# Kernel optimization log

Measured on AMD Instinct MI355X. Metric: run time of the kernel, lower is better.

The kernel has to match this reference:

```python
import jax, jax.numpy as jnp
import numpy as np

NUM_GROUPS = 32
EPS = 1e-6
NUM_HEADS = 8
HEAD_DIM = 64


def group_norm(x, gamma, beta):
    # x: [B, C, H, W]
    B, C, H, W = x.shape
    xg = x.reshape(B, NUM_GROUPS, C // NUM_GROUPS, H, W)
    mean = xg.mean(axis=(2, 3, 4), keepdims=True)
    var = xg.var(axis=(2, 3, 4), keepdims=True)
    xn = ((xg - mean) * jax.lax.rsqrt(var + EPS)).reshape(B, C, H, W)
    return xn * gamma[None, :, None, None] + beta[None, :, None, None]


def setup_inputs() -> dict:
    key = jax.random.key(0)
    ks = jax.random.split(key, 4)
    B, C, H, W = 8, 512, 32, 32
    hid = NUM_HEADS * HEAD_DIM  # 512
    x = jax.random.normal(ks[0], (B, C, H, W), dtype=jnp.float32)
    gamma = jnp.ones((C,), dtype=jnp.float32)
    beta = jnp.zeros((C,), dtype=jnp.float32)
    w_in = jax.random.normal(ks[1], (3 * hid, C), dtype=jnp.float32) * (1.0 / np.sqrt(C))
    b_in = jnp.zeros((3 * hid,), dtype=jnp.float32)
    w_out = jax.random.normal(ks[2], (C, hid), dtype=jnp.float32) * (1.0 / np.sqrt(hid))
    b_out = jnp.zeros((C,), dtype=jnp.float32)
    return {"x": x, "gamma": gamma, "beta": beta, "w_in": w_in, "b_in": b_in,
            "w_out": w_out, "b_out": b_out}


def reference(x, gamma, beta, w_in, b_in, w_out, b_out):
    B, C, H, W = x.shape
    n, c = NUM_HEADS, HEAD_DIM
    skip = x
    h = group_norm(x, gamma, beta)
    # 1x1 conv proj_in: [B, 3*n*c, H, W]
    qkv = jnp.einsum('oc,bchw->bohw', w_in, h) + b_in[None, :, None, None]
    qkv = qkv.reshape(B, 3, n, c, H * W)
    q, k, v = qkv[:, 0], qkv[:, 1], qkv[:, 2]  # each [B, n, c, HW]
    scale = 1.0 / np.sqrt(c)
    logits = jnp.einsum('bncq,bnck->bnqk', q, k) * scale  # [B, n, HW, HW]
    w = jax.nn.softmax(logits, axis=-1)
    out = jnp.einsum('bnqk,bnck->bncq', w, v)  # [B, n, c, HW]
    out = out.reshape(B, n * c, H, W)
    out = jnp.einsum('oc,bchw->bohw', w_out, out) + b_out[None, :, None, None]
    return out + skip
```

## Files before the change

### kernel.cpp

```cpp
#include <hip/hip_runtime.h>
#include <hip/hip_bf16.h>

#define B_    8
#define C_    512
#define HW_   1024
#define NG    32
#define GCH   16
#define EPSV  1e-6f

typedef __attribute__((ext_vector_type(8))) short short8;
typedef __attribute__((ext_vector_type(4))) short short4v;
typedef __attribute__((ext_vector_type(4))) float floatx4;

static __device__ __forceinline__ short f2bs(float f) {
  return __builtin_bit_cast(short, __float2bfloat16(f));
}
static __device__ __forceinline__ short4v pack4(float a, float b, float c, float d) {
  return (short4v){f2bs(a), f2bs(b), f2bs(c), f2bs(d)};
}
static __device__ __forceinline__ unsigned pk2(float a, float b) {
  return (unsigned)(unsigned short)f2bs(a) |
         ((unsigned)(unsigned short)f2bs(b) << 16);
}
#define MFMA(a, b, c) __builtin_amdgcn_mfma_f32_16x16x32_bf16((a), (b), (c), 0, 0, 0)

static __device__ __forceinline__ void glds16(const short* g, short* l) {
  __builtin_amdgcn_global_load_lds(
      (const __attribute__((address_space(1))) void*)g,
      (__attribute__((address_space(3))) void*)l, 16, 0, 0);
}

__global__ __launch_bounds__(256) void cast2_f2b(
    const float* __restrict__ s1, short* __restrict__ d1,
    const float* __restrict__ s2, short* __restrict__ d2) {
  int i = blockIdx.x * 256 + threadIdx.x;
  const float* s; short* d; int j;
  if (i < 196608) { s = s1; d = d1; j = i; }
  else            { s = s2; d = d2; j = i - 196608; }
  float4 v = reinterpret_cast<const float4*>(s)[j];
  reinterpret_cast<short4v*>(d)[j] = pack4(v.x, v.y, v.z, v.w);
}

__global__ __launch_bounds__(256) void gn_stats(
    const float* __restrict__ x, float2* __restrict__ stats) {
  int bg = blockIdx.x;
  const int n = GCH * HW_;
  const float* xp = x + (size_t)bg * n;
  int t = threadIdx.x;

  float s = 0.f, ss = 0.f;
  for (int i = t; i < n / 4; i += 256) {
    float4 v = *reinterpret_cast<const float4*>(xp + i * 4);
    s  += (v.x + v.y) + (v.z + v.w);
    ss += (v.x * v.x + v.y * v.y) + (v.z * v.z + v.w * v.w);
  }
  for (int o = 32; o > 0; o >>= 1) {
    s  += __shfl_down(s, o);
    ss += __shfl_down(ss, o);
  }
  __shared__ float rs_[4], rss_[4];
  int wid = t >> 6, lane = t & 63;
  if (lane == 0) { rs_[wid] = s; rss_[wid] = ss; }
  __syncthreads();
  if (t == 0) {
    float stot  = rs_[0] + rs_[1] + rs_[2] + rs_[3];
    float sstot = rss_[0] + rss_[1] + rss_[2] + rss_[3];
    float mean = stot / (float)n;
    float var  = sstot / (float)n - mean * mean;
    stats[bg] = make_float2(mean, rsqrtf(var + EPSV));
  }
}

__global__ __launch_bounds__(256) void gn_apply(
    const float* __restrict__ x, const float2* __restrict__ stats,
    const float* __restrict__ gamma, const float* __restrict__ beta,
    short* __restrict__ ht) {
  __shared__ float Ls[64 * 65];
  int s0 = blockIdx.x * 64, ch0 = blockIdx.y * 64, b = blockIdx.z;
  int t = threadIdx.x;

  for (int i = 0; i < 4; i++) {
    int lin = t + i * 256;
    int r = lin >> 4, c4 = lin & 15;
    int ch = ch0 + r;
    float2 st = stats[b * NG + (ch >> 4)];
    float ga = gamma[ch] * st.y;
    float be = beta[ch] - st.x * ga;
    float4 v = *reinterpret_cast<const float4*>(
        x + ((size_t)(b * C_ + ch)) * HW_ + s0 + c4 * 4);
    Ls[r * 65 + c4 * 4 + 0] = v.x * ga + be;
    Ls[r * 65 + c4 * 4 + 1] = v.y * ga + be;
    Ls[r * 65 + c4 * 4 + 2] = v.z * ga + be;
    Ls[r * 65 + c4 * 4 + 3] = v.w * ga + be;
  }
  __syncthreads();
  for (int i = 0; i < 4; i++) {
    int lin = t + i * 256;
    int sq = lin >> 4, cq = lin & 15;
    float a0 = Ls[(cq * 4 + 0) * 65 + sq];
    float a1 = Ls[(cq * 4 + 1) * 65 + sq];
    float a2 = Ls[(cq * 4 + 2) * 65 + sq];
    float a3 = Ls[(cq * 4 + 3) * 65 + sq];
    *reinterpret_cast<short4v*>(
        ht + ((size_t)b * 1024 + s0 + sq) * 512 + ch0 + cq * 4) =
        pack4(a0, a1, a2, a3);
  }
}

__global__ __launch_bounds__(256) void gemm_qkv(
    const short* __restrict__ Wb, const short* __restrict__ ht,
    const float* __restrict__ bias,
    short* __restrict__ Qt, short* __restrict__ Kt, short* __restrict__ Vn) {
  __shared__ short As[2][4096];
  __shared__ short Bs[2][4096];
  int bx = blockIdx.x, by = blockIdx.y, bb = blockIdx.z;
  int m0 = by * 128, n0 = bx * 128;
  int t = threadIdx.x;
  int w = t >> 6, lane = t & 63, n16 = lane & 15, quad = lane >> 4;
  int wm = (w >> 1) * 64, wn = (w & 1) * 64;

  const short* Wa = Wb + (size_t)(m0 + (t >> 2)) * 512 + (t & 3) * 8;
  const short* Xa = ht + (size_t)bb * 1024 * 512 +
                    (size_t)(n0 + (t >> 2)) * 512 + (t & 3) * 8;

#define STAGE(buf, kk)                                                \
  do {                                                                \
    glds16(Wa + (kk), &As[buf][t * 8]);                               \
    glds16(Wa + 64 * 512 + (kk), &As[buf][2048 + t * 8]);             \
    glds16(Xa + (kk), &Bs[buf][t * 8]);                               \
    glds16(Xa + 64 * 512 + (kk), &Bs[buf][2048 + t * 8]);             \
  } while (0)

  floatx4 acc[4][4];
  for (int i = 0; i < 4; i++)
    for (int j = 0; j < 4; j++) acc[i][j] = (floatx4){0.f, 0.f, 0.f, 0.f};

  STAGE(0, 0);
#pragma unroll 1
  for (int ks = 0; ks < 16; ks++) {
    int cur = ks & 1;
    __syncthreads();
    if (ks < 15) STAGE(cur ^ 1, (ks + 1) * 32);
    short8 a[4], b[4];
    for (int im = 0; im < 4; im++)
      a[im] = *reinterpret_cast<const short8*>(
          &As[cur][(wm + im * 16 + n16) * 32 + quad * 8]);
    for (int in = 0; in < 4; in++)
      b[in] = *reinterpret_cast<const short8*>(
          &Bs[cur][(wn + in * 16 + n16) * 32 + quad * 8]);
    for (int im = 0; im < 4; im++)
      for (int in = 0; in < 4; in++)
        acc[im][in] = MFMA(a[im], b[in], acc[im][in]);
  }
#undef STAGE

  if (m0 < 1024) {
    const bool isQ = (m0 < 512);
    short* base = isQ ? Qt : Kt;
    const float sc = isQ ? 0.125f : 1.0f;
    for (int im = 0; im < 4; im++) {
      int m = m0 + wm + im * 16 + quad * 4;
      int hh = (m >> 6) & 7, d0 = m & 63;
      float4 bi = *reinterpret_cast<const float4*>(&bias[m]);
      short* hb = base + (size_t)(bb * 8 + hh) * 1024 * 64 + d0;
      for (int in = 0; in < 4; in++) {
        int nn = n0 + wn + in * 16 + n16;
        *reinterpret_cast<short4v*>(hb + (size_t)nn * 64) =
            pack4((acc[im][in][0] + bi.x) * sc, (acc[im][in][1] + bi.y) * sc,
                  (acc[im][in][2] + bi.z) * sc, (acc[im][in][3] + bi.w) * sc);
      }
    }
  } else {
    for (int im = 0; im < 4; im++) {
      int m = m0 + wm + im * 16 + quad * 4;
      float4 bi = *reinterpret_cast<const float4*>(&bias[m]);
      int ch = m - 1024;
      for (int in = 0; in < 4; in++) {
        int nn = n0 + wn + in * 16 + n16;
        short* vp = Vn + (size_t)(bb * 512 + ch) * 1024 + nn;
        vp[0]    = f2bs(acc[im][in][0] + bi.x);
        vp[1024] = f2bs(acc[im][in][1] + bi.y);
        vp[2048] = f2bs(acc[im][in][2] + bi.z);
        vp[3072] = f2bs(acc[im][in][3] + bi.w);
      }
    }
  }
}

__global__ __launch_bounds__(256) void attn_mfma(
    const short* __restrict__ Qt, const short* __restrict__ Kt,
    const short* __restrict__ Vn, short* __restrict__ attnT) {
  int blk0 = blockIdx.x;
  int blk = (blk0 & 7) * 64 + (blk0 >> 3);
  int qb = blk & 7, h = (blk >> 3) & 7, b = blk >> 6;
  int t = threadIdx.x;
  int w = t >> 6, lane = t & 63, n16 = lane & 15, quad = lane >> 4;
  int q0 = qb * 128 + w * 32;
  int qhi = quad >> 1;
  int srcA = ((quad & 1) << 5) + n16;
  int srcB = srcA + 16;

  const short* Qp = Qt + (size_t)(b * 8 + h) * 1024 * 64;
  const short* Kp = Kt + (size_t)(b * 8 + h) * 1024 * 64;
  const short* Vp = Vn + (size_t)(b * 512 + h * 64) * 1024;

  short8 qa[2][2];
  for (int qt = 0; qt < 2; qt++)
    for (int f = 0; f < 2; f++)
      qa[qt][f] = *reinterpret_cast<const short8*>(
          Qp + (size_t)(q0 + qt * 16 + n16) * 64 + f * 32 + quad * 8);

  floatx4 O[2][4];
  float l[2] = {0.f, 0.f};
  for (int qt = 0; qt < 2; qt++)
    for (int i = 0; i < 4; i++) O[qt][i] = (floatx4){0.f, 0.f, 0.f, 0.f};

#define LOADK(dst, ktv)                                                      \
  do {                                                                       \
    int k0_ = (ktv) * 64;                                                    \
    for (int nt_ = 0; nt_ < 4; nt_++)                                        \
      for (int f_ = 0; f_ < 2; f_++)                                         \
        dst[nt_][f_] = *reinterpret_cast<const short8*>(                     \
            Kp + (size_t)(k0_ + nt_ * 16 + n16) * 64 + f_ * 32 + quad * 8);  \
  } while (0)

#define BODY(kf, ktv)                                                        \
  do {                                                                       \
    int k0_ = (ktv) * 64;                                                    \
      \
    short8 v_[4][2];                                                         \
    for (int nd_ = 0; nd_ < 4; nd_++) {                                      \
      const short* vs_ =                                                     \
          Vp + (size_t)(nd_ * 16 + n16) * 1024 + k0_ + quad * 8;             \
      v_[nd_][0] = *reinterpret_cast<const short8*>(vs_);                    \
      v_[nd_][1] = *reinterpret_cast<const short8*>(vs_ + 32);               \
    }                                                                        \
    _Pragma("unroll")                                                        \
    for (int qt_ = 0; qt_ < 2; qt_++) {                                      \
               \
      floatx4 T_[4];                                                         \
      _Pragma("unroll")                                                      \
      for (int nt_ = 0; nt_ < 4; nt_++) {                                    \
        floatx4 s_ = (floatx4){0.f, 0.f, 0.f, 0.f};                          \
        s_ = MFMA(kf[nt_][0], qa[qt_][0], s_);                               \
        T_[nt_] = MFMA(kf[nt_][1], qa[qt_][1], s_);                          \
      }                                                                      \
      unsigned u_[4][2];                                                     \
      _Pragma("unroll")                                                      \
      for (int nt_ = 0; nt_ < 4; nt_++) {                                    \
        float p0_ = __expf(T_[nt_][0]);                                      \
        float p1_ = __expf(T_[nt_][1]);                                      \
        float p2_ = __expf(T_[nt_][2]);                                      \
        float p3_ = __expf(T_[nt_][3]);                                      \
        l[qt_] += (p0_ + p1_) + (p2_ + p3_);                                 \
        u_[nt_][0] = pk2(p0_, p1_);                                         \
        u_[nt_][1] = pk2(p2_, p3_);                                         \
      }                                                                      \
                         \
      short8 pa_[2];                                                         \
      _Pragma("unroll")                                                      \
      for (int f_ = 0; f_ < 2; f_++) {                                       \
        unsigned a0_ = (unsigned)__shfl((int)u_[2 * f_ + 0][0], srcA);       \
        unsigned a1_ = (unsigned)__shfl((int)u_[2 * f_ + 1][0], srcA);       \
        unsigned b0_ = (unsigned)__shfl((int)u_[2 * f_ + 0][1], srcA);       \
        unsigned b1_ = (unsigned)__shfl((int)u_[2 * f_ + 1][1], srcA);       \
        unsigned c0_ = (unsigned)__shfl((int)u_[2 * f_ + 0][0], srcB);       \
        unsigned c1_ = (unsigned)__shfl((int)u_[2 * f_ + 1][0], srcB);       \
        unsigned d0_ = (unsigned)__shfl((int)u_[2 * f_ + 0][1], srcB);       \
        unsigned d1_ = (unsigned)__shfl((int)u_[2 * f_ + 1][1], srcB);       \
        uint4 wv_;                                                           \
        wv_.x = qhi ? a1_ : a0_;                                             \
        wv_.y = qhi ? b1_ : b0_;                                             \
        wv_.z = qhi ? c1_ : c0_;                                             \
        wv_.w = qhi ? d1_ : d0_;                                             \
        pa_[f_] = __builtin_bit_cast(short8, wv_);                           \
      }                                                                      \
      __builtin_amdgcn_s_setprio(1);                                         \
      _Pragma("unroll")                                                      \
      for (int nd_ = 0; nd_ < 4; nd_++) {                                    \
        O[qt_][nd_] = MFMA(pa_[0], v_[nd_][0], O[qt_][nd_]);                 \
        O[qt_][nd_] = MFMA(pa_[1], v_[nd_][1], O[qt_][nd_]);                 \
      }                                                                      \
      __builtin_amdgcn_s_setprio(0);                                         \
    }                                                                        \
  } while (0)

  short8 kfA[4][2], kfB[4][2];
  LOADK(kfA, 0);
#pragma unroll 1
  for (int kt = 0; kt < 16; kt += 2) {
    LOADK(kfB, kt + 1);
    BODY(kfA, kt);
    if (kt + 2 < 16) LOADK(kfA, kt + 2);
    BODY(kfB, kt + 1);
  }
#undef LOADK
#undef BODY

  for (int qt = 0; qt < 2; qt++) {
    float s = l[qt];
    s += __shfl_xor(s, 16);
    s += __shfl_xor(s, 32);
    for (int nd = 0; nd < 4; nd++)
      for (int r = 0; r < 4; r++) {
        float linv = 1.0f / __shfl(s, quad * 4 + r);
        int q = q0 + qt * 16 + quad * 4 + r;
        int ch = h * 64 + nd * 16 + n16;
        attnT[((size_t)b * 1024 + q) * 512 + ch] = f2bs(O[qt][nd][r] * linv);
      }
  }
}

__global__ __launch_bounds__(256) void gemm_out(
    const short* __restrict__ Wb, const short* __restrict__ Xt,
    const float* __restrict__ bias, const float* __restrict__ resid,
    float* __restrict__ out) {
  __shared__ short As[2][2048];
  __shared__ short Bs[2][2048];
  int bx = blockIdx.x, by = blockIdx.y, bb = blockIdx.z;
  int m0 = by * 64, n0 = bx * 64;
  int t = threadIdx.x;
  int w = t >> 6, lane = t & 63, n16 = lane & 15, quad = lane >> 4;
  int wm = (w >> 1) * 32, wn = (w & 1) * 32;

  const short* Wa = Wb + (size_t)(m0 + (t >> 2)) * 512 + (t & 3) * 8;
  const short* Xa = Xt + (size_t)bb * 1024 * 512 +
                    (size_t)(n0 + (t >> 2)) * 512 + (t & 3) * 8;

#define STAGE(buf, kk)                                                \
  do {                                                                \
    glds16(Wa + (kk), &As[buf][t * 8]);                               \
    glds16(Xa + (kk), &Bs[buf][t * 8]);                               \
  } while (0)

  floatx4 acc[2][2];
  for (int i = 0; i < 2; i++)
    for (int j = 0; j < 2; j++) acc[i][j] = (floatx4){0.f, 0.f, 0.f, 0.f};

  STAGE(0, 0);
#pragma unroll 1
  for (int ks = 0; ks < 16; ks++) {
    int cur = ks & 1;
    __syncthreads();
    if (ks < 15) STAGE(cur ^ 1, (ks + 1) * 32);
    short8 a[2], b[2];
    for (int im = 0; im < 2; im++)
      a[im] = *reinterpret_cast<const short8*>(
          &As[cur][(wm + im * 16 + n16) * 32 + quad * 8]);
    for (int in = 0; in < 2; in++)
      b[in] = *reinterpret_cast<const short8*>(
          &Bs[cur][(wn + in * 16 + n16) * 32 + quad * 8]);
    for (int im = 0; im < 2; im++)
      for (int in = 0; in < 2; in++)
        acc[im][in] = MFMA(a[im], b[in], acc[im][in]);
  }
#undef STAGE

  for (int im = 0; im < 2; im++) {
    int m = m0 + wm + im * 16 + quad * 4;
    float4 bi = *reinterpret_cast<const float4*>(&bias[m]);
    for (int in = 0; in < 2; in++) {
      int nn = n0 + wn + in * 16 + n16;
      size_t idx = ((size_t)bb * 512 + m) * 1024 + nn;
      out[idx]        = acc[im][in][0] + bi.x + resid[idx];
      out[idx + 1024] = acc[im][in][1] + bi.y + resid[idx + 1024];
      out[idx + 2048] = acc[im][in][2] + bi.z + resid[idx + 2048];
      out[idx + 3072] = acc[im][in][3] + bi.w + resid[idx + 3072];
    }
  }
}

extern "C" void kernel_launch(void* const* d_in, const int* in_sizes, int n_in,
                              void* d_out, int out_size, void* d_ws, size_t ws_size,
                              hipStream_t stream) {
  const float* x     = (const float*)d_in[0];
  const float* gamma = (const float*)d_in[1];
  const float* beta  = (const float*)d_in[2];
  const float* w_in  = (const float*)d_in[3];
  const float* b_in  = (const float*)d_in[4];
  const float* w_out = (const float*)d_in[5];
  const float* b_out = (const float*)d_in[6];
  float* out = (float*)d_out;

  char* ws = (char*)d_ws;
  short* ht    = (short*)ws;
  short* Qt    = (short*)(ws + (8u  << 20));
  short* Kt    = (short*)(ws + (16u << 20));
  short* Vn    = (short*)(ws + (24u << 20));
  short* attnT = (short*)(ws + (32u << 20));
  short* wbf1  = (short*)(ws + (40u << 20));
  short* wbf2  = (short*)(ws + (42u << 20));
  float2* stats = (float2*)(ws + (44u << 20));

  cast2_f2b<<<1024, 256, 0, stream>>>(w_in, wbf1, w_out, wbf2);
  gn_stats<<<B_ * NG, 256, 0, stream>>>(x, stats);
  gn_apply<<<dim3(16, 8, B_), 256, 0, stream>>>(x, stats, gamma, beta, ht);
  gemm_qkv<<<dim3(8, 12, B_), 256, 0, stream>>>(wbf1, ht, b_in, Qt, Kt, Vn);
  attn_mfma<<<512, 256, 0, stream>>>(Qt, Kt, Vn, attnT);
  gemm_out<<<dim3(16, 8, B_), 256, 0, stream>>>(wbf2, attnT, b_out, x, out);
}
```

Measured before the change: 191.7 us.

## Software-pipeline attention QK, softmax and PV phases across key tiles

Splits the attention inner loop body into separate QK, softmax and PV phases and interleaves them across two key tiles. The QK MFMAs of the next tile now overlap with the exp/shuffle work of the current one, and K is prefetched two tiles ahead. It also pins the kernel to 2 waves per EU, which gives each wave a larger register budget for the extra live fragments. In exchange, occupancy drops and register pressure rises, which may reduce latency hiding or cause spills.

```diff
diff --git a/kernel.cpp b/kernel.cpp
--- a/kernel.cpp
+++ b/kernel.cpp
@@ -187,7 +187,8 @@
   }
 }
 
-__global__ __launch_bounds__(256) void attn_mfma(
+__global__ __launch_bounds__(256)
+__attribute__((amdgpu_waves_per_eu(2, 2))) void attn_mfma(
     const short* __restrict__ Qt, const short* __restrict__ Kt,
     const short* __restrict__ Vn, short* __restrict__ attnT) {
   int blk0 = blockIdx.x;
@@ -224,40 +225,45 @@
             Kp + (size_t)(k0_ + nt_ * 16 + n16) * 64 + f_ * 32 + quad * 8);  \
   } while (0)
 
-#define BODY(kf, ktv)                                                        \
+#define LOADV(dst, ktv)                                                      \
   do {                                                                       \
     int k0_ = (ktv) * 64;                                                    \
-      \
-    short8 v_[4][2];                                                         \
     for (int nd_ = 0; nd_ < 4; nd_++) {                                      \
       const short* vs_ =                                                     \
           Vp + (size_t)(nd_ * 16 + n16) * 1024 + k0_ + quad * 8;             \
-      v_[nd_][0] = *reinterpret_cast<const short8*>(vs_);                    \
-      v_[nd_][1] = *reinterpret_cast<const short8*>(vs_ + 32);               \
+      dst[nd_][0] = *reinterpret_cast<const short8*>(vs_);                   \
+      dst[nd_][1] = *reinterpret_cast<const short8*>(vs_ + 32);              \
     }                                                                        \
+  } while (0)
+
+#define QKPH(kf, T)                                                          \
+  do {                                                                       \
     _Pragma("unroll")                                                        \
     for (int qt_ = 0; qt_ < 2; qt_++) {                                      \
-               \
-      floatx4 T_[4];                                                         \
       _Pragma("unroll")                                                      \
       for (int nt_ = 0; nt_ < 4; nt_++) {                                    \
         floatx4 s_ = (floatx4){0.f, 0.f, 0.f, 0.f};                          \
         s_ = MFMA(kf[nt_][0], qa[qt_][0], s_);                               \
-        T_[nt_] = MFMA(kf[nt_][1], qa[qt_][1], s_);                          \
+        T[qt_][nt_] = MFMA(kf[nt_][1], qa[qt_][1], s_);                      \
       }                                                                      \
+    }                                                                        \
+  } while (0)
+
+#define SMAX(T, pa)                                                          \
+  do {                                                                       \
+    _Pragma("unroll")                                                        \
+    for (int qt_ = 0; qt_ < 2; qt_++) {                                      \
       unsigned u_[4][2];                                                     \
       _Pragma("unroll")                                                      \
       for (int nt_ = 0; nt_ < 4; nt_++) {                                    \
-        float p0_ = __expf(T_[nt_][0]);                                      \
-        float p1_ = __expf(T_[nt_][1]);                                      \
-        float p2_ = __expf(T_[nt_][2]);                                      \
-        float p3_ = __expf(T_[nt_][3]);                                      \
+        float p0_ = __expf(T[qt_][nt_][0]);                                  \
+        float p1_ = __expf(T[qt_][nt_][1]);                                  \
+        float p2_ = __expf(T[qt_][nt_][2]);                                  \
+        float p3_ = __expf(T[qt_][nt_][3]);                                  \
         l[qt_] += (p0_ + p1_) + (p2_ + p3_);                                 \
-        u_[nt_][0] = pk2(p0_, p1_);                                         \
-        u_[nt_][1] = pk2(p2_, p3_);                                         \
+        u_[nt_][0] = pk2(p0_, p1_);                                          \
+        u_[nt_][1] = pk2(p2_, p3_);                                          \
       }                                                                      \
-                         \
-      short8 pa_[2];                                                         \
       _Pragma("unroll")                                                      \
       for (int f_ = 0; f_ < 2; f_++) {                                       \
         unsigned a0_ = (unsigned)__shfl((int)u_[2 * f_ + 0][0], srcA);       \
@@ -273,29 +279,48 @@
         wv_.y = qhi ? b1_ : b0_;                                             \
         wv_.z = qhi ? c1_ : c0_;                                             \
         wv_.w = qhi ? d1_ : d0_;                                             \
-        pa_[f_] = __builtin_bit_cast(short8, wv_);                           \
+        pa[qt_][f_] = __builtin_bit_cast(short8, wv_);                       \
       }                                                                      \
-      __builtin_amdgcn_s_setprio(1);                                         \
+    }                                                                        \
+  } while (0)
+
+#define PVPH(pa, v)                                                          \
+  do {                                                                       \
+    __builtin_amdgcn_s_setprio(1);                                           \
+    _Pragma("unroll")                                                        \
+    for (int qt_ = 0; qt_ < 2; qt_++) {                                      \
       _Pragma("unroll")                                                      \
       for (int nd_ = 0; nd_ < 4; nd_++) {                                    \
-        O[qt_][nd_] = MFMA(pa_[0], v_[nd_][0], O[qt_][nd_]);                 \
-        O[qt_][nd_] = MFMA(pa_[1], v_[nd_][1], O[qt_][nd_]);                 \
+        O[qt_][nd_] = MFMA(pa[qt_][0], v[nd_][0], O[qt_][nd_]);              \
+        O[qt_][nd_] = MFMA(pa[qt_][1], v[nd_][1], O[qt_][nd_]);              \
       }                                                                      \
-      __builtin_amdgcn_s_setprio(0);                                         \
     }                                                                        \
+    __builtin_amdgcn_s_setprio(0);                                           \
   } while (0)
 
   short8 kfA[4][2], kfB[4][2];
   LOADK(kfA, 0);
+  LOADK(kfB, 1);
 #pragma unroll 1
   for (int kt = 0; kt < 16; kt += 2) {
-    LOADK(kfB, kt + 1);
-    BODY(kfA, kt);
+    floatx4 TA[2][4], TB[2][4];
+    short8 vA[4][2], vB[4][2], paA[2][2], paB[2][2];
+    QKPH(kfA, TA);
     if (kt + 2 < 16) LOADK(kfA, kt + 2);
-    BODY(kfB, kt + 1);
+    LOADV(vA, kt);
+    SMAX(TA, paA);
+    QKPH(kfB, TB);
+    if (kt + 3 < 16) LOADK(kfB, kt + 3);
+    PVPH(paA, vA);
+    LOADV(vB, kt + 1);
+    SMAX(TB, paB);
+    PVPH(paB, vB);
   }
 #undef LOADK
-#undef BODY
+#undef LOADV
+#undef QKPH
+#undef SMAX
+#undef PVPH
 
   for (int qt = 0; qt < 2; qt++) {
     float s = l[qt];
```

After: 190.3 us. About the same (-0.8%).

## Fuse group-norm stats, apply, and weight casts into one kernel

Applied to the files above, without the earlier changes.

Merges the weight cast, group-norm statistics and group-norm apply/transpose kernels into one launch. Each of the 256 blocks handles one (batch, group) pair: it computes the statistics, then re-reads its 64KB slice (likely cache-resident) to normalize and transpose it into bf16. The remaining blocks do the weight casts. This removes two launches and the stats round trip through memory. In exchange the transposed writes are only 16 channels wide (32-byte chunks), and each block runs 16 sequential tiles with two barriers per tile, so there is less parallelism than the old 1024-block apply kernel.

```diff
diff --git a/kernel.cpp b/kernel.cpp
--- a/kernel.cpp
+++ b/kernel.cpp
@@ -30,27 +30,33 @@
       (__attribute__((address_space(3))) void*)l, 16, 0, 0);
 }
 
-__global__ __launch_bounds__(256) void cast2_f2b(
-    const float* __restrict__ s1, short* __restrict__ d1,
-    const float* __restrict__ s2, short* __restrict__ d2) {
-  int i = blockIdx.x * 256 + threadIdx.x;
-  const float* s; short* d; int j;
-  if (i < 196608) { s = s1; d = d1; j = i; }
-  else            { s = s2; d = d2; j = i - 196608; }
-  float4 v = reinterpret_cast<const float4*>(s)[j];
-  reinterpret_cast<short4v*>(d)[j] = pack4(v.x, v.y, v.z, v.w);
-}
-
-__global__ __launch_bounds__(256) void gn_stats(
-    const float* __restrict__ x, float2* __restrict__ stats) {
-  int bg = blockIdx.x;
-  const int n = GCH * HW_;
-  const float* xp = x + (size_t)bg * n;
+__global__ __launch_bounds__(256) void gn_cast_fused(
+    const float* __restrict__ x, const float* __restrict__ gamma,
+    const float* __restrict__ beta, short* __restrict__ ht,
+    const float* __restrict__ w_in, short* __restrict__ wbf1,
+    const float* __restrict__ w_out, short* __restrict__ wbf2) {
+  int blk = blockIdx.x;
   int t = threadIdx.x;
 
+  if (blk >= 256) {
+    int i = (blk - 256) * 256 + t;
+    const float* s; short* d; int j;
+    if (i < 196608) { s = w_in; d = wbf1; j = i; }
+    else            { s = w_out; d = wbf2; j = i - 196608; }
+    float4 v = reinterpret_cast<const float4*>(s)[j];
+    reinterpret_cast<short4v*>(d)[j] = pack4(v.x, v.y, v.z, v.w);
+    return;
+  }
+
+  int b = blk >> 5, g = blk & 31;
+  const float* xp = x + ((size_t)(b * C_) + g * GCH) * HW_;
+
+  __shared__ float Ls[16 * 65];
+  __shared__ float rs_[4], rss_[4], st_[2];
+
   float s = 0.f, ss = 0.f;
-  for (int i = t; i < n / 4; i += 256) {
-    float4 v = *reinterpret_cast<const float4*>(xp + i * 4);
+  for (int i = 0; i < 16; i++) {
+    float4 v = *reinterpret_cast<const float4*>(xp + (t + i * 256) * 4);
     s  += (v.x + v.y) + (v.z + v.w);
     ss += (v.x * v.x + v.y * v.y) + (v.z * v.z + v.w * v.w);
   }
@@ -58,52 +64,41 @@
     s  += __shfl_down(s, o);
     ss += __shfl_down(ss, o);
   }
-  __shared__ float rs_[4], rss_[4];
   int wid = t >> 6, lane = t & 63;
   if (lane == 0) { rs_[wid] = s; rss_[wid] = ss; }
   __syncthreads();
   if (t == 0) {
     float stot  = rs_[0] + rs_[1] + rs_[2] + rs_[3];
     float sstot = rss_[0] + rss_[1] + rss_[2] + rss_[3];
-    float mean = stot / (float)n;
-    float var  = sstot / (float)n - mean * mean;
-    stats[bg] = make_float2(mean, rsqrtf(var + EPSV));
-  }
-}
-
-__global__ __launch_bounds__(256) void gn_apply(
-    const float* __restrict__ x, const float2* __restrict__ stats,
-    const float* __restrict__ gamma, const float* __restrict__ beta,
-    short* __restrict__ ht) {
-  __shared__ float Ls[64 * 65];
-  int s0 = blockIdx.x * 64, ch0 = blockIdx.y * 64, b = blockIdx.z;
-  int t = threadIdx.x;
-
-  for (int i = 0; i < 4; i++) {
-    int lin = t + i * 256;
-    int r = lin >> 4, c4 = lin & 15;
-    int ch = ch0 + r;
-    float2 st = stats[b * NG + (ch >> 4)];
-    float ga = gamma[ch] * st.y;
-    float be = beta[ch] - st.x * ga;
-    float4 v = *reinterpret_cast<const float4*>(
-        x + ((size_t)(b * C_ + ch)) * HW_ + s0 + c4 * 4);
+    float mean = stot / 16384.f;
+    float var  = sstot / 16384.f - mean * mean;
+    st_[0] = mean;
+    st_[1] = rsqrtf(var + EPSV);
+  }
+  __syncthreads();
+
+  int r = t >> 4, c4 = t & 15;
+  int ch = g * GCH + r;
+  float ga = gamma[ch] * st_[1];
+  float be = beta[ch] - st_[0] * ga;
+  int sq = t >> 2, cq = t & 3;
+
+  for (int stile = 0; stile < 16; stile++) {
+    int s0 = stile * 64;
+    float4 v = *reinterpret_cast<const float4*>(xp + r * HW_ + s0 + c4 * 4);
     Ls[r * 65 + c4 * 4 + 0] = v.x * ga + be;
     Ls[r * 65 + c4 * 4 + 1] = v.y * ga + be;
     Ls[r * 65 + c4 * 4 + 2] = v.z * ga + be;
     Ls[r * 65 + c4 * 4 + 3] = v.w * ga + be;
-  }
-  __syncthreads();
-  for (int i = 0; i < 4; i++) {
-    int lin = t + i * 256;
-    int sq = lin >> 4, cq = lin & 15;
+    __syncthreads();
     float a0 = Ls[(cq * 4 + 0) * 65 + sq];
     float a1 = Ls[(cq * 4 + 1) * 65 + sq];
     float a2 = Ls[(cq * 4 + 2) * 65 + sq];
     float a3 = Ls[(cq * 4 + 3) * 65 + sq];
     *reinterpret_cast<short4v*>(
-        ht + ((size_t)b * 1024 + s0 + sq) * 512 + ch0 + cq * 4) =
+        ht + ((size_t)b * 1024 + s0 + sq) * 512 + g * GCH + cq * 4) =
         pack4(a0, a1, a2, a3);
+    __syncthreads();
   }
 }
 
@@ -227,7 +222,6 @@
 #define BODY(kf, ktv)                                                        \
   do {                                                                       \
     int k0_ = (ktv) * 64;                                                    \
-      \
     short8 v_[4][2];                                                         \
     for (int nd_ = 0; nd_ < 4; nd_++) {                                      \
       const short* vs_ =                                                     \
@@ -237,7 +231,6 @@
     }                                                                        \
     _Pragma("unroll")                                                        \
     for (int qt_ = 0; qt_ < 2; qt_++) {                                      \
-               \
       floatx4 T_[4];                                                         \
       _Pragma("unroll")                                                      \
       for (int nt_ = 0; nt_ < 4; nt_++) {                                    \
@@ -256,7 +249,6 @@
         u_[nt_][0] = pk2(p0_, p1_);                                         \
         u_[nt_][1] = pk2(p2_, p3_);                                         \
       }                                                                      \
-                         \
       short8 pa_[2];                                                         \
       _Pragma("unroll")                                                      \
       for (int f_ = 0; f_ < 2; f_++) {                                       \
@@ -390,11 +382,9 @@
   short* attnT = (short*)(ws + (32u << 20));
   short* wbf1  = (short*)(ws + (40u << 20));
   short* wbf2  = (short*)(ws + (42u << 20));
-  float2* stats = (float2*)(ws + (44u << 20));
-
-  cast2_f2b<<<1024, 256, 0, stream>>>(w_in, wbf1, w_out, wbf2);
-  gn_stats<<<B_ * NG, 256, 0, stream>>>(x, stats);
-  gn_apply<<<dim3(16, 8, B_), 256, 0, stream>>>(x, stats, gamma, beta, ht);
+
+  gn_cast_fused<<<1280, 256, 0, stream>>>(x, gamma, beta, ht,
+                                          w_in, wbf1, w_out, wbf2);
   gemm_qkv<<<dim3(8, 12, B_), 256, 0, stream>>>(wbf1, ht, b_in, Qt, Kt, Vn);
   attn_mfma<<<512, 256, 0, stream>>>(Qt, Kt, Vn, attnT);
   gemm_out<<<dim3(16, 8, B_), 256, 0, stream>>>(wbf2, attnT, b_out, x, out);
```

After: 188.2 us. No clear change (-1.8%).
